# Kernel tuning notes

Measured on AMD Instinct MI355X. Metric: run time of the kernel, lower is better.

The kernel has to match this reference:

```python
import jax, jax.numpy as jnp
import numpy as np

B, S, H = 4, 8192, 768
NH, HD = 12, 64          # num_heads, head_size
M = 64                   # projection_dim = min(256, HD)
EPS = 1e-6

def setup_inputs() -> dict:
    key = jax.random.key(0)
    ks = jax.random.split(key, 10)
    scale_w = 0.02
    scale_p = 1.0 / np.sqrt(HD)
    return {
        'hidden_states': jax.random.normal(ks[0], (B, S, H), jnp.float32),
        'Wq': jax.random.normal(ks[1], (H, H), jnp.float32) * scale_w,
        'bq': jnp.zeros((H,), jnp.float32),
        'Wk': jax.random.normal(ks[2], (H, H), jnp.float32) * scale_w,
        'bk': jnp.zeros((H,), jnp.float32),
        'Wv': jax.random.normal(ks[3], (H, H), jnp.float32) * scale_w,
        'bv': jnp.zeros((H,), jnp.float32),
        'Wo': jax.random.normal(ks[4], (H, H), jnp.float32) * scale_w,
        'bo': jnp.zeros((H,), jnp.float32),
        'projection_matrix': jax.random.normal(ks[5], (NH, HD, M), jnp.float32) * scale_p,
    }

def reference(hidden_states, Wq, bq, Wk, bk, Wv, bv, Wo, bo, projection_matrix):
    b, s, h = hidden_states.shape
    def heads(x):  # [b,s,h] -> [b,nh,s,hd]
        return x.reshape(b, s, NH, HD).transpose(0, 2, 1, 3)
    q = heads(hidden_states @ Wq + bq)
    k = heads(hidden_states @ Wk + bk)
    v = heads(hidden_states @ Wv + bv)
    # random-feature projection + stabilized exp feature map
    qp = jnp.einsum('bhnd,hdm->bhnm', q, projection_matrix)
    kp = jnp.einsum('bhnd,hdm->bhnm', k, projection_matrix)
    qp = jnp.exp(qp - jnp.max(qp, axis=-1, keepdims=True))
    kp = jnp.exp(kp - jnp.max(kp, axis=-1, keepdims=True))
    # O(n) linear attention: kv summary [b,h,m,hd]
    kv = jnp.einsum('bhnm,bhnd->bhmd', kp, v)
    qkv = jnp.einsum('bhnm,bhmd->bhnd', qp, kv)
    k_sum = jnp.sum(kp, axis=2)                      # [b,h,m]
    normalizer = jnp.einsum('bhnm,bhm->bhn', qp, k_sum)[..., None]
    ctx = qkv / (normalizer + EPS)
    ctx = ctx.transpose(0, 2, 1, 3).reshape(b, s, NH * HD)
    return ctx @ Wo + bo
```

## Files before the change

kernel.cpp:

```cpp
#include <hip/hip_runtime.h>
#include <hip/hip_bf16.h>


#define S_    8192
#define H_    768
#define NH_   12
#define EPS_  1e-6f

typedef unsigned short U16;
typedef short bf16x8 __attribute__((ext_vector_type(8)));
typedef float f32x4  __attribute__((ext_vector_type(4)));

__device__ __forceinline__ U16 f2b(float x) {
  unsigned u = __float_as_uint(x);
  return (U16)((u + 0x7fffu + ((u >> 16) & 1u)) >> 16);
}
__device__ __forceinline__ float b2f(U16 h) {
  return __uint_as_float(((unsigned)h) << 16);
}
__device__ __forceinline__ void gl2lds16(const void* g, void* l) {
  __builtin_amdgcn_global_load_lds(
      (const __attribute__((address_space(1))) void*)g,
      (__attribute__((address_space(3))) void*)l, 16, 0, 0);
}

__global__ void zero_f32(float* __restrict__ p, int n) {
  int i = blockIdx.x * 256 + threadIdx.x;
  if (i < n) p[i] = 0.f;
}

__global__ void cvt_f32_bf16(const float* __restrict__ src, U16* __restrict__ hi, int n4) {
  int i = blockIdx.x * 256 + threadIdx.x;
  if (i >= n4) return;
  float4 x = ((const float4*)src)[i];
  ushort4 h;
  h.x = f2b(x.x); h.y = f2b(x.y); h.z = f2b(x.z); h.w = f2b(x.w);
  ((ushort4*)hi)[i] = h;
}

__global__ void fold_proj(const float* __restrict__ Wq, const float* __restrict__ bq,
                          const float* __restrict__ Wk, const float* __restrict__ bk,
                          const float* __restrict__ P,
                          float* __restrict__ Wqp, float* __restrict__ bqp,
                          float* __restrict__ Wkp, float* __restrict__ bkp) {
  __shared__ float Pl[64 * 64];
  __shared__ float WL[4 * 64];
  int h = blockIdx.y, kc = blockIdx.x, tid = threadIdx.x;
  const float* W  = blockIdx.z ? Wk : Wq;
  const float* bb = blockIdx.z ? bk : bq;
  float* Wout = blockIdx.z ? Wkp : Wqp;
  float* bout = blockIdx.z ? bkp : bqp;
  const float4* P4 = (const float4*)(P + (size_t)h * 4096);
#pragma unroll
  for (int i = 0; i < 4; ++i) ((float4*)Pl)[tid + i * 256] = P4[tid + i * 256];
  WL[tid] = W[(size_t)(kc * 4 + (tid >> 6)) * H_ + h * 64 + (tid & 63)];
  __syncthreads();
  int kl = tid >> 6, m = tid & 63;
  float acc = 0.f;
#pragma unroll
  for (int d = 0; d < 64; ++d) acc += WL[kl * 64 + d] * Pl[d * 64 + m];
  Wout[(size_t)(kc * 4 + kl) * H_ + h * 64 + m] = acc;
  if (kc == 0 && tid < 64) {
    float a2 = 0.f;
    for (int d = 0; d < 64; ++d) a2 += bb[h * 64 + d] * Pl[d * 64 + tid];
    bout[h * 64 + tid] = a2;
  }
}

__global__ void build_cat_t(const float* __restrict__ Wqp, const float* __restrict__ Wkp,
                            const float* __restrict__ Wv,  const float* __restrict__ Wo,
                            U16* __restrict__ WcatH, U16* __restrict__ WoTH) {
  __shared__ float T[64][68];
  const int kb = blockIdx.x, rb = blockIdx.y, mat = blockIdx.z;
  const int tid = threadIdx.x;
  const float* W = mat == 0 ? Wqp : (mat == 1 ? Wkp : (mat == 2 ? Wv : Wo));
#pragma unroll
  for (int p = 0; p < 4; ++p) {
    int idx = tid + p * 256;
    int rr = idx >> 4, c4 = (idx & 15) * 4;
    float4 v = *(const float4*)&W[(size_t)(kb * 64 + rr) * H_ + rb * 64 + c4];
    T[rr][c4] = v.x; T[rr][c4 + 1] = v.y; T[rr][c4 + 2] = v.z; T[rr][c4 + 3] = v.w;
  }
  __syncthreads();
  U16* dst = mat == 3 ? WoTH : WcatH;
  const int rbase = (mat == 3 ? 0 : mat * 768) + rb * 64;
#pragma unroll
  for (int p = 0; p < 4; ++p) {
    int idx = tid + p * 256;
    int r2 = idx >> 4, c2 = (idx & 15) * 4;
    ushort4 o;
    o.x = f2b(T[c2 + 0][r2]); o.y = f2b(T[c2 + 1][r2]);
    o.z = f2b(T[c2 + 2][r2]); o.w = f2b(T[c2 + 3][r2]);
    *(ushort4*)&dst[(size_t)(rbase + r2) * H_ + kb * 64 + c2] = o;
  }
}

__global__ void build_bias(const float* __restrict__ bqp, const float* __restrict__ bkp,
                           const float* __restrict__ bv, float* __restrict__ biasC) {
  int i = blockIdx.x * 256 + threadIdx.x;
  if (i >= 2304) return;
  biasC[i] = i < 768 ? bqp[i] : (i < 1536 ? bkp[i - 768] : bv[i - 1536]);
}

__global__ __launch_bounds__(256, 2) void gemm_qkv(
    const U16* __restrict__ Ahi, const U16* __restrict__ Bhi,
    const float* __restrict__ bias,
    U16* __restrict__ qp, U16* __restrict__ kpT, U16* __restrict__ vT,
    float* __restrict__ ksumF) {
  __shared__ __align__(16) U16 Us[32768];
  const int tid = threadIdx.x, w = tid >> 6, lane = tid & 63;
  const int quad = lane >> 4, l16 = lane & 15;
  const int b = blockIdx.x;
  const int mt = b & 255, nt0 = b >> 8;
  const int rowA0 = mt * 128;
  const int wm = w & 1, wn = w >> 1;
  const U16* srcA[4];
  int rowBl[4];
  unsigned ldsc[4];
  const int kch = ((lane & 7) ^ (lane >> 3)) * 8;
#pragma unroll
  for (int t = 0; t < 4; ++t) {
    int c = w * 4 + t;
    int row = c * 8 + (lane >> 3);
    srcA[t] = Ahi + (size_t)(rowA0 + row) * H_ + kch;
    rowBl[t] = row;
    ldsc[t] = (unsigned)c * 512;
  }
  auto stage = [&](int jn, int tn, int bi) {
    const int colB = (nt0 + 2 * jn) * 128;
    unsigned ub = (unsigned)bi * 16384u;
#pragma unroll
    for (int t = 0; t < 4; ++t) {
      gl2lds16(srcA[t] + tn * 64, &Us[ub + ldsc[t]]);
      gl2lds16(Bhi + (size_t)(colB + rowBl[t]) * H_ + tn * 64 + kch,
               &Us[ub + 8192u + ldsc[t]]);
    }
  };

  stage(0, 0, 0);
  for (int jj = 0; jj < 9; ++jj) {
    const int colB0 = (nt0 + 2 * jj) * 128;
    f32x4 acc[4][4] = {};
    for (int t = 0; t < 12; ++t) {
      const bool more = !(jj == 8 && t == 11);
      if (more) {
        if (t < 11) stage(jj, t + 1, (t + 1) & 1);
        else        stage(jj + 1, 0, 0);
        asm volatile("s_waitcnt vmcnt(8)" ::: "memory");
      } else {
        asm volatile("s_waitcnt vmcnt(0)" ::: "memory");
      }
      __builtin_amdgcn_sched_barrier(0);
      __builtin_amdgcn_s_barrier();
      __builtin_amdgcn_sched_barrier(0);
      const unsigned ab = (unsigned)(t & 1) * 16384u;
      bf16x8 ah[4][2], bh[4][2];
#pragma unroll
      for (int i = 0; i < 4; ++i)
#pragma unroll
        for (int ks = 0; ks < 2; ++ks)
          ah[i][ks] = *(const bf16x8*)&Us[ab +
              (unsigned)((wm * 64 + i * 16 + l16) * 64 +
                         (((ks * 4 + quad) ^ (l16 & 7)) * 8))];
#pragma unroll
      for (int j = 0; j < 4; ++j)
#pragma unroll
        for (int ks = 0; ks < 2; ++ks)
          bh[j][ks] = *(const bf16x8*)&Us[ab + 8192u +
              (unsigned)((wn * 64 + j * 16 + l16) * 64 +
                         (((ks * 4 + quad) ^ (l16 & 7)) * 8))];
      asm volatile("s_waitcnt lgkmcnt(0)" ::: "memory");
      __builtin_amdgcn_sched_barrier(0);
      __builtin_amdgcn_s_setprio(1);
#pragma unroll
      for (int ks = 0; ks < 2; ++ks)
#pragma unroll
        for (int j = 0; j < 4; ++j)
#pragma unroll
          for (int i = 0; i < 4; ++i)
            acc[i][j] = __builtin_amdgcn_mfma_f32_16x16x32_bf16(
                ah[i][ks], bh[j][ks], acc[i][j], 0, 0, 0);
      __builtin_amdgcn_s_setprio(0);
      __builtin_amdgcn_sched_barrier(0);
      __builtin_amdgcn_s_barrier();
      __builtin_amdgcn_sched_barrier(0);
    }
    const int col64 = colB0 + wn * 64;
    float bj[4];
#pragma unroll
    for (int j = 0; j < 4; ++j) bj[j] = bias[col64 + j * 16 + l16];
    if (col64 < 768) {
      const int h = col64 >> 6;
#pragma unroll
      for (int i = 0; i < 4; ++i) {
#pragma unroll
        for (int r = 0; r < 4; ++r) {
          int row = rowA0 + wm * 64 + i * 16 + quad * 4 + r;
          float v0 = acc[i][0][r] + bj[0], v1 = acc[i][1][r] + bj[1];
          float v2 = acc[i][2][r] + bj[2], v3 = acc[i][3][r] + bj[3];
          float mx = fmaxf(fmaxf(v0, v1), fmaxf(v2, v3));
          mx = fmaxf(mx, __shfl_xor(mx, 1));
          mx = fmaxf(mx, __shfl_xor(mx, 2));
          mx = fmaxf(mx, __shfl_xor(mx, 4));
          mx = fmaxf(mx, __shfl_xor(mx, 8));
          int bb = row >> 13, s = row & 8191;
          size_t base = ((size_t)(bb * NH_ + h) * S_ + s) * 64 + l16;
          qp[base +  0] = f2b(__expf(v0 - mx));
          qp[base + 16] = f2b(__expf(v1 - mx));
          qp[base + 32] = f2b(__expf(v2 - mx));
          qp[base + 48] = f2b(__expf(v3 - mx));
        }
      }
    } else {
      const int isv = col64 >= 1536;
      const int h = (col64 - (isv ? 1536 : 768)) >> 6;
      U16* dstT = isv ? vT : kpT;
      const int bh2 = (rowA0 >> 13) * NH_ + h;
      float pk[4] = {0.f, 0.f, 0.f, 0.f};
#pragma unroll
      for (int i = 0; i < 4; ++i) {
        float er[4][4];
#pragma unroll
        for (int r = 0; r < 4; ++r) {
          float v0 = acc[i][0][r] + bj[0], v1 = acc[i][1][r] + bj[1];
          float v2 = acc[i][2][r] + bj[2], v3 = acc[i][3][r] + bj[3];
          if (!isv) {
            float mx = fmaxf(fmaxf(v0, v1), fmaxf(v2, v3));
            mx = fmaxf(mx, __shfl_xor(mx, 1));
            mx = fmaxf(mx, __shfl_xor(mx, 2));
            mx = fmaxf(mx, __shfl_xor(mx, 4));
            mx = fmaxf(mx, __shfl_xor(mx, 8));
            v0 = __expf(v0 - mx); v1 = __expf(v1 - mx);
            v2 = __expf(v2 - mx); v3 = __expf(v3 - mx);
          }
          er[0][r] = v0; er[1][r] = v1; er[2][r] = v2; er[3][r] = v3;
        }
        if (!isv) {
#pragma unroll
          for (int j = 0; j < 4; ++j)
            pk[j] += er[j][0] + er[j][1] + er[j][2] + er[j][3];
        }
        int n = rowA0 + wm * 64 + i * 16 + quad * 4;
        int s = n & 8191;
#pragma unroll
        for (int j = 0; j < 4; ++j) {
          ushort4 o;
          o.x = f2b(er[j][0]); o.y = f2b(er[j][1]);
          o.z = f2b(er[j][2]); o.w = f2b(er[j][3]);
          *(ushort4*)&dstT[((size_t)bh2 * 64 + j * 16 + l16) * S_ + s] = o;
        }
      }
      if (!isv) {
#pragma unroll
        for (int j = 0; j < 4; ++j) {
          pk[j] += __shfl_xor(pk[j], 16);
          pk[j] += __shfl_xor(pk[j], 32);
        }
        if (quad == 0) {
#pragma unroll
          for (int j = 0; j < 4; ++j)
            atomicAdd(&ksumF[bh2 * 64 + j * 16 + l16], pk[j]);
        }
      }
    }
  }
}

__global__ __launch_bounds__(256, 4) void kv_accum_mfma(
    const U16* __restrict__ kpT, const U16* __restrict__ vT,
    float* __restrict__ kvM) {
  __shared__ __align__(16) U16 Us[2 * 64 * 64];
  const int tid = threadIdx.x, w = tid >> 6, lane = tid & 63;
  const int quad = lane >> 4, l16 = lane & 15;
  const int bh = blockIdx.y;
  const int n0 = blockIdx.x * 512;
  const U16* srcs[4];
  unsigned ldsoff[4];
#pragma unroll
  for (int t = 0; t < 4; ++t) {
    int c = w * 4 + t, buf = c >> 3;
    int r = (c & 7) * 8 + (lane >> 3);
    const U16* base = buf ? kpT : vT;
    srcs[t] = base + ((size_t)bh * 64 + r) * S_ + n0 + (lane & 7) * 8;
    ldsoff[t] = buf * 4096 + (c & 7) * 512;
  }
  f32x4 acc[4] = {};
  for (int nc = 0; nc < 512; nc += 64) {
#pragma unroll
    for (int t = 0; t < 4; ++t) gl2lds16(srcs[t] + nc, &Us[ldsoff[t]]);
    __syncthreads();
#pragma unroll
    for (int k0 = 0; k0 < 64; k0 += 32) {
      bf16x8 av = *(const bf16x8*)&Us[(w * 16 + l16) * 64 + k0 + quad * 8];
#pragma unroll
      for (int j = 0; j < 4; ++j) {
        bf16x8 bk = *(const bf16x8*)&Us[4096 + (j * 16 + l16) * 64 + k0 + quad * 8];
        acc[j] = __builtin_amdgcn_mfma_f32_16x16x32_bf16(av, bk, acc[j], 0, 0, 0);
      }
    }
    __syncthreads();
  }
#pragma unroll
  for (int j = 0; j < 4; ++j)
#pragma unroll
    for (int r = 0; r < 4; ++r)
      atomicAdd(&kvM[((size_t)bh * 64 + j * 16 + l16) * 64 + w * 16 + quad * 4 + r],
                acc[j][r]);
}

__global__ __launch_bounds__(256) void wkv_build(
    const float* __restrict__ kvM, const U16* __restrict__ WoTH,
    U16* __restrict__ WKVT) {
  __shared__ float kvL[64][65];
  __shared__ U16  WoL[128][66];
  const int tid = threadIdx.x;
  const int cB = blockIdx.x * 128, bh = blockIdx.y;
  const int b = bh / NH_, h = bh - b * NH_;
#pragma unroll
  for (int p = 0; p < 16; ++p) {
    int idx = tid + p * 256;
    kvL[idx >> 6][idx & 63] = kvM[(size_t)bh * 4096 + idx];
  }
#pragma unroll
  for (int p = 0; p < 32; ++p) {
    int idx = tid + p * 256;
    WoL[idx >> 6][idx & 63] = WoTH[(size_t)(cB + (idx >> 6)) * H_ + h * 64 + (idx & 63)];
  }
  __syncthreads();
  const int c = tid & 127, m0 = (tid >> 7) * 32;
  float acc[32] = {};
  for (int d = 0; d < 64; ++d) {
    float wv = b2f(WoL[c][d]);
#pragma unroll
    for (int mm = 0; mm < 32; ++mm) acc[mm] += wv * kvL[m0 + mm][d];
  }
  U16* dst = WKVT + (size_t)b * 589824 + (size_t)(cB + c) * H_ + h * 64 + m0;
#pragma unroll
  for (int mm = 0; mm < 32; mm += 4) {
    ushort4 o;
    o.x = f2b(acc[mm]); o.y = f2b(acc[mm + 1]);
    o.z = f2b(acc[mm + 2]); o.w = f2b(acc[mm + 3]);
    *(ushort4*)&dst[mm] = o;
  }
}

__global__ __launch_bounds__(256) void qpn_scale(
    const U16* __restrict__ qp, const float* __restrict__ ksumF,
    U16* __restrict__ ctx) {
  __shared__ float ks[64];
  const int tid = threadIdx.x;
  const int bh = blockIdx.y, s0 = blockIdx.x * 64;
  if (tid < 64) ks[tid] = ksumF[bh * 64 + tid];
  __syncthreads();
  const int row = tid >> 2, q = tid & 3;
  size_t src = ((size_t)bh * S_ + s0 + row) * 64 + q * 16;
  bf16x8 x0 = *(const bf16x8*)&qp[src];
  bf16x8 x1 = *(const bf16x8*)&qp[src + 8];
  float f[16];
  float n = 0.f;
#pragma unroll
  for (int e = 0; e < 8; ++e) {
    f[e] = b2f((U16)x0[e]);     n += f[e] * ks[q * 16 + e];
    f[e + 8] = b2f((U16)x1[e]); n += f[e + 8] * ks[q * 16 + 8 + e];
  }
  n += __shfl_xor(n, 1);
  n += __shfl_xor(n, 2);
  const float inv = 1.f / (n + EPS_);
  const int b = bh / NH_, h = bh - b * NH_;
  U16* dst = ctx + ((size_t)(b * S_ + s0 + row)) * H_ + h * 64 + q * 16;
#pragma unroll
  for (int g = 0; g < 4; ++g) {
    ushort4 o;
    o.x = f2b(f[g * 4 + 0] * inv); o.y = f2b(f[g * 4 + 1] * inv);
    o.z = f2b(f[g * 4 + 2] * inv); o.w = f2b(f[g * 4 + 3] * inv);
    *(ushort4*)&dst[g * 4] = o;
  }
}

__global__ __launch_bounds__(256, 4) void out_gemm(
    const U16* __restrict__ Ahi, const U16* __restrict__ WKVT,
    const float* __restrict__ bias, float* __restrict__ C) {
  __shared__ __align__(16) U16 Us[2 * 128 * 32];
  const int tid = threadIdx.x, w = tid >> 6, lane = tid & 63;
  const int quad = lane >> 4, l16 = lane & 15;
  const int rowA0 = blockIdx.y * 128, colB0 = blockIdx.x * 128;
  const int wm = w & 1, wn = w >> 1;
  const int K = 768;
  const U16* Bb = WKVT + (size_t)(blockIdx.y >> 6) * 589824;
  f32x4 acc[4][4] = {};
  const U16* srcs[4];
  unsigned ldsoff[4];
#pragma unroll
  for (int t = 0; t < 4; ++t) {
    int c = w * 4 + t, cc = c & 7, buf = c >> 3;
    const U16* base = buf ? Bb : Ahi;
    int r0 = buf ? colB0 : rowA0;
    srcs[t] = base + (size_t)(r0 + cc * 16 + (lane >> 2)) * K + (lane & 3) * 8;
    ldsoff[t] = c * 512;
  }
  for (int k0 = 0; k0 < K; k0 += 32) {
#pragma unroll
    for (int t = 0; t < 4; ++t) gl2lds16(srcs[t] + k0, &Us[ldsoff[t]]);
    __syncthreads();
    bf16x8 ah[4];
#pragma unroll
    for (int i = 0; i < 4; ++i)
      ah[i] = *(const bf16x8*)&Us[(wm * 64 + i * 16 + l16) * 32 + quad * 8];
#pragma unroll
    for (int j = 0; j < 4; ++j) {
      bf16x8 bh = *(const bf16x8*)&Us[4096 + (wn * 64 + j * 16 + l16) * 32 + quad * 8];
#pragma unroll
      for (int i = 0; i < 4; ++i)
        acc[i][j] = __builtin_amdgcn_mfma_f32_16x16x32_bf16(ah[i], bh, acc[i][j], 0, 0, 0);
    }
    __syncthreads();
  }
#pragma unroll
  for (int i = 0; i < 4; ++i) {
    int row = rowA0 + wm * 64 + i * 16 + quad * 4;
#pragma unroll
    for (int j = 0; j < 4; ++j) {
      int col = colB0 + wn * 64 + j * 16 + l16;
      float bvv = bias[col];
#pragma unroll
      for (int r = 0; r < 4; ++r)
        C[(size_t)(row + r) * H_ + col] = acc[i][j][r] + bvv;
    }
  }
}

extern "C" void kernel_launch(void* const* d_in, const int* in_sizes, int n_in,
                              void* d_out, int out_size, void* d_ws, size_t ws_size,
                              hipStream_t stream) {
  const float* hs = (const float*)d_in[0];
  const float* Wq = (const float*)d_in[1];
  const float* bq = (const float*)d_in[2];
  const float* Wk = (const float*)d_in[3];
  const float* bk = (const float*)d_in[4];
  const float* Wv = (const float*)d_in[5];
  const float* bv = (const float*)d_in[6];
  const float* Wo = (const float*)d_in[7];
  const float* bo = (const float*)d_in[8];
  const float* P  = (const float*)d_in[9];
  float* out = (float*)d_out;

  char* ws = (char*)d_ws;
  size_t off = 0;
  auto alloc = [&](size_t bytes) -> void* {
    void* p = ws + off;
    off = (off + bytes + 255) & ~(size_t)255;
    return p;
  };
  U16*   hs_hi = (U16*)alloc(50331648);
  float* WqpF  = (float*)alloc(2359296);
  float* WkpF  = (float*)alloc(2359296);
  float* bqpF  = (float*)alloc(3072);
  float* bkpF  = (float*)alloc(3072);
  U16*   WcatH = (U16*)alloc(3538944);
  U16*   WoTH  = (U16*)alloc(1179648);
  float* biasC = (float*)alloc(9216);
  U16*   qp    = (U16*)alloc(50331648);
  U16*   kpT   = (U16*)alloc(50331648);
  U16*   vT    = (U16*)alloc(50331648);
  float* kvM   = (float*)alloc(786432);
  float* ksumF = (float*)alloc(12288);
  U16*   WKVT  = (U16*)alloc(4718592);
  U16*   ctx   = hs_hi;

  zero_f32<<<dim3(780), dim3(256), 0, stream>>>(kvM, 199680);
  cvt_f32_bf16<<<dim3(24576), dim3(256), 0, stream>>>(hs, hs_hi, 6291456);
  fold_proj<<<dim3(192, 12, 2), dim3(256), 0, stream>>>(Wq, bq, Wk, bk, P, WqpF, bqpF, WkpF, bkpF);
  build_cat_t<<<dim3(12, 12, 4), dim3(256), 0, stream>>>(WqpF, WkpF, Wv, Wo, WcatH, WoTH);
  build_bias<<<dim3(9), dim3(256), 0, stream>>>(bqpF, bkpF, bv, biasC);
  gemm_qkv<<<dim3(512), dim3(256), 0, stream>>>(hs_hi, WcatH, biasC, qp, kpT, vT, ksumF);
  kv_accum_mfma<<<dim3(16, 48), dim3(256), 0, stream>>>(kpT, vT, kvM);
  wkv_build<<<dim3(6, 48), dim3(256), 0, stream>>>(kvM, WoTH, WKVT);
  qpn_scale<<<dim3(128, 48), dim3(256), 0, stream>>>(qp, ksumF, ctx);
  out_gemm<<<dim3(6, 256), dim3(256), 0, stream>>>(ctx, WKVT, bo, out);
}
```

Measured before the change: 549.1 us.

## Read head-major normalized qp directly in out_gemm with double-buffered swizzled LDS

qpn_scale now normalizes qp in place instead of scattering it into a token-major ctx buffer. out_gemm reads the head-major qp layout directly, with each K step of 64 mapped to one head. It also double-buffers LDS tiles with XOR swizzling, explicit waitcnt/barrier pipelining and setprio around MFMAs, and makes each block loop over three N tiles so the grid shrinks to 512 blocks. This cuts strided writes and overlaps global-to-LDS loads with compute, at the cost of more LDS per block and lower occupancy.

```diff
diff --git a/kernel.cpp b/kernel.cpp
--- a/kernel.cpp
+++ b/kernel.cpp
@@ -345,8 +345,7 @@
 }
 
 __global__ __launch_bounds__(256) void qpn_scale(
-    const U16* __restrict__ qp, const float* __restrict__ ksumF,
-    U16* __restrict__ ctx) {
+    U16* __restrict__ qp, const float* __restrict__ ksumF) {
   __shared__ float ks[64];
   const int tid = threadIdx.x;
   const int bh = blockIdx.y, s0 = blockIdx.x * 64;
@@ -366,65 +365,107 @@
   n += __shfl_xor(n, 1);
   n += __shfl_xor(n, 2);
   const float inv = 1.f / (n + EPS_);
-  const int b = bh / NH_, h = bh - b * NH_;
-  U16* dst = ctx + ((size_t)(b * S_ + s0 + row)) * H_ + h * 64 + q * 16;
 #pragma unroll
   for (int g = 0; g < 4; ++g) {
     ushort4 o;
     o.x = f2b(f[g * 4 + 0] * inv); o.y = f2b(f[g * 4 + 1] * inv);
     o.z = f2b(f[g * 4 + 2] * inv); o.w = f2b(f[g * 4 + 3] * inv);
-    *(ushort4*)&dst[g * 4] = o;
-  }
-}
-
-__global__ __launch_bounds__(256, 4) void out_gemm(
-    const U16* __restrict__ Ahi, const U16* __restrict__ WKVT,
-    const float* __restrict__ bias, float* __restrict__ C) {
-  __shared__ __align__(16) U16 Us[2 * 128 * 32];
+    *(ushort4*)&qp[src + g * 4] = o;
+  }
+}
+
+__global__ __launch_bounds__(256, 2) void out_gemm(
+    const U16* __restrict__ qpn, const U16* __restrict__ WKVT,
+    const float* __restrict__ bo, float* __restrict__ out) {
+  __shared__ __align__(16) U16 Us[32768];
   const int tid = threadIdx.x, w = tid >> 6, lane = tid & 63;
   const int quad = lane >> 4, l16 = lane & 15;
-  const int rowA0 = blockIdx.y * 128, colB0 = blockIdx.x * 128;
+  const int b = blockIdx.x;
+  const int mt = b & 255, nt0 = b >> 8;
+  const int rowA0 = mt * 128;
+  const int batch = mt >> 6, s0 = (mt & 63) * 128;
+  const int bh0 = batch * NH_;
   const int wm = w & 1, wn = w >> 1;
-  const int K = 768;
-  const U16* Bb = WKVT + (size_t)(blockIdx.y >> 6) * 589824;
-  f32x4 acc[4][4] = {};
-  const U16* srcs[4];
-  unsigned ldsoff[4];
+  const int kch = ((lane & 7) ^ (lane >> 3)) * 8;
+  int rowc[4];
+  unsigned ldsc[4];
 #pragma unroll
   for (int t = 0; t < 4; ++t) {
-    int c = w * 4 + t, cc = c & 7, buf = c >> 3;
-    const U16* base = buf ? Bb : Ahi;
-    int r0 = buf ? colB0 : rowA0;
-    srcs[t] = base + (size_t)(r0 + cc * 16 + (lane >> 2)) * K + (lane & 3) * 8;
-    ldsoff[t] = c * 512;
-  }
-  for (int k0 = 0; k0 < K; k0 += 32) {
-#pragma unroll
-    for (int t = 0; t < 4; ++t) gl2lds16(srcs[t] + k0, &Us[ldsoff[t]]);
-    __syncthreads();
-    bf16x8 ah[4];
-#pragma unroll
-    for (int i = 0; i < 4; ++i)
-      ah[i] = *(const bf16x8*)&Us[(wm * 64 + i * 16 + l16) * 32 + quad * 8];
-#pragma unroll
-    for (int j = 0; j < 4; ++j) {
-      bf16x8 bh = *(const bf16x8*)&Us[4096 + (wn * 64 + j * 16 + l16) * 32 + quad * 8];
+    rowc[t] = (w * 4 + t) * 8 + (lane >> 3);
+    ldsc[t] = (unsigned)(w * 4 + t) * 512;
+  }
+  const U16* wb = WKVT + (size_t)batch * 589824;
+  auto stage = [&](int jn, int tn, int bi) {
+    const int colB = (nt0 * 3 + jn) * 128;
+    unsigned ub = (unsigned)bi * 16384u;
+    const U16* abase = qpn + ((size_t)(bh0 + tn) * S_ + s0) * 64 + kch;
+    const U16* bbase = wb + (size_t)colB * H_ + tn * 64 + kch;
+#pragma unroll
+    for (int t = 0; t < 4; ++t) {
+      gl2lds16(abase + rowc[t] * 64, &Us[ub + ldsc[t]]);
+      gl2lds16(bbase + (size_t)rowc[t] * H_, &Us[ub + 8192u + ldsc[t]]);
+    }
+  };
+
+  stage(0, 0, 0);
+  for (int jj = 0; jj < 3; ++jj) {
+    const int colB0 = (nt0 * 3 + jj) * 128;
+    f32x4 acc[4][4] = {};
+    for (int t = 0; t < 12; ++t) {
+      const bool more = !(jj == 2 && t == 11);
+      if (more) {
+        if (t < 11) stage(jj, t + 1, (t + 1) & 1);
+        else        stage(jj + 1, 0, 0);
+        asm volatile("s_waitcnt vmcnt(8)" ::: "memory");
+      } else {
+        asm volatile("s_waitcnt vmcnt(0)" ::: "memory");
+      }
+      __builtin_amdgcn_sched_barrier(0);
+      __builtin_amdgcn_s_barrier();
+      __builtin_amdgcn_sched_barrier(0);
+      const unsigned ab = (unsigned)(t & 1) * 16384u;
+      bf16x8 ah[4][2], bh[4][2];
 #pragma unroll
       for (int i = 0; i < 4; ++i)
-        acc[i][j] = __builtin_amdgcn_mfma_f32_16x16x32_bf16(ah[i], bh, acc[i][j], 0, 0, 0);
-    }
-    __syncthreads();
-  }
-#pragma unroll
-  for (int i = 0; i < 4; ++i) {
-    int row = rowA0 + wm * 64 + i * 16 + quad * 4;
-#pragma unroll
-    for (int j = 0; j < 4; ++j) {
-      int col = colB0 + wn * 64 + j * 16 + l16;
-      float bvv = bias[col];
-#pragma unroll
-      for (int r = 0; r < 4; ++r)
-        C[(size_t)(row + r) * H_ + col] = acc[i][j][r] + bvv;
+#pragma unroll
+        for (int ks = 0; ks < 2; ++ks)
+          ah[i][ks] = *(const bf16x8*)&Us[ab +
+              (unsigned)((wm * 64 + i * 16 + l16) * 64 +
+                         (((ks * 4 + quad) ^ (l16 & 7)) * 8))];
+#pragma unroll
+      for (int j = 0; j < 4; ++j)
+#pragma unroll
+        for (int ks = 0; ks < 2; ++ks)
+          bh[j][ks] = *(const bf16x8*)&Us[ab + 8192u +
+              (unsigned)((wn * 64 + j * 16 + l16) * 64 +
+                         (((ks * 4 + quad) ^ (l16 & 7)) * 8))];
+      asm volatile("s_waitcnt lgkmcnt(0)" ::: "memory");
+      __builtin_amdgcn_sched_barrier(0);
+      __builtin_amdgcn_s_setprio(1);
+#pragma unroll
+      for (int ks = 0; ks < 2; ++ks)
+#pragma unroll
+        for (int j = 0; j < 4; ++j)
+#pragma unroll
+          for (int i = 0; i < 4; ++i)
+            acc[i][j] = __builtin_amdgcn_mfma_f32_16x16x32_bf16(
+                ah[i][ks], bh[j][ks], acc[i][j], 0, 0, 0);
+      __builtin_amdgcn_s_setprio(0);
+      __builtin_amdgcn_sched_barrier(0);
+      __builtin_amdgcn_s_barrier();
+      __builtin_amdgcn_sched_barrier(0);
+    }
+#pragma unroll
+    for (int i = 0; i < 4; ++i) {
+      int row = rowA0 + wm * 64 + i * 16 + quad * 4;
+#pragma unroll
+      for (int j = 0; j < 4; ++j) {
+        int col = colB0 + wn * 64 + j * 16 + l16;
+        float bvv = bo[col];
+#pragma unroll
+        for (int r = 0; r < 4; ++r)
+          out[(size_t)(row + r) * H_ + col] = acc[i][j][r] + bvv;
+      }
     }
   }
 }
@@ -465,7 +506,6 @@
   float* kvM   = (float*)alloc(786432);
   float* ksumF = (float*)alloc(12288);
   U16*   WKVT  = (U16*)alloc(4718592);
-  U16*   ctx   = hs_hi;
 
   zero_f32<<<dim3(780), dim3(256), 0, stream>>>(kvM, 199680);
   cvt_f32_bf16<<<dim3(24576), dim3(256), 0, stream>>>(hs, hs_hi, 6291456);
@@ -475,6 +515,6 @@
   gemm_qkv<<<dim3(512), dim3(256), 0, stream>>>(hs_hi, WcatH, biasC, qp, kpT, vT, ksumF);
   kv_accum_mfma<<<dim3(16, 48), dim3(256), 0, stream>>>(kpT, vT, kvM);
   wkv_build<<<dim3(6, 48), dim3(256), 0, stream>>>(kvM, WoTH, WKVT);
-  qpn_scale<<<dim3(128, 48), dim3(256), 0, stream>>>(qp, ksumF, ctx);
-  out_gemm<<<dim3(6, 256), dim3(256), 0, stream>>>(ctx, WKVT, bo, out);
-}
+  qpn_scale<<<dim3(128, 48), dim3(256), 0, stream>>>(qp, ksumF);
+  out_gemm<<<dim3(512), dim3(256), 0, stream>>>(qp, WKVT, bo, out);
+}
```

After: 518.6 us. 1.06x faster.
